# Performance work log

Measured on AMD Instinct MI355X. Metric: run time of the kernel, lower is better.

The kernel has to match this reference:

```python
import jax, jax.numpy as jnp
import numpy as np

NUM_HEADS = 12
KEEP_RATE = 0.7


def setup_inputs() -> dict:
    key = jax.random.key(0)
    ks = jax.random.split(key, 5)
    B, N, C = 64, 197, 768
    x = jax.random.normal(ks[0], (B, N, C), dtype=jnp.float32)
    qkv_w = jax.random.normal(ks[1], (3 * C, C), dtype=jnp.float32) * (C ** -0.5)
    qkv_b = jax.random.normal(ks[2], (3 * C,), dtype=jnp.float32) * 0.02
    proj_w = jax.random.normal(ks[3], (C, C), dtype=jnp.float32) * (C ** -0.5)
    proj_b = jax.random.normal(ks[4], (C,), dtype=jnp.float32) * 0.02
    return {"x": x, "qkv_w": qkv_w, "qkv_b": qkv_b, "proj_w": proj_w, "proj_b": proj_b}


def reference(x, qkv_w, qkv_b, proj_w, proj_b):
    B, N, C = x.shape
    H = NUM_HEADS
    D = C // H
    scale = D ** -0.5
    # qkv projection: [B,N,3C] -> [3,B,H,N,D]
    qkv = (x @ qkv_w.T + qkv_b).reshape(B, N, 3, H, D).transpose(2, 0, 3, 1, 4)
    q, k, v = qkv[0], qkv[1], qkv[2]
    # full materialized attention (required for cls-row extraction)
    attn = jax.nn.softmax(jnp.einsum('bhqd,bhkd->bhqk', q, k) * scale, axis=-1)
    out = jnp.einsum('bhqk,bhkd->bqhd', attn, v).reshape(B, N, C)
    out = out @ proj_w.T + proj_b
    # EViT token pruning: cls-token attention over non-cls keys, head-averaged
    left_tokens = int(KEEP_RATE * (N - 1))  # 137
    cls_attn = attn[:, :, 0, 1:].mean(axis=1)  # [B, N-1]
    _, idx = jax.lax.top_k(cls_attn, left_tokens)  # sorted descending, like torch.topk
    index = jnp.broadcast_to(idx[:, :, None], (B, left_tokens, C))
    return (out, index, idx, cls_attn)
```

## Files before the change

### kernel.cpp

```cpp
#include <hip/hip_runtime.h>
#include <hip/hip_bf16.h>
#include <stdint.h>

constexpr int BATCH = 64;
constexpr int NTOK  = 197;
constexpr int CDIM  = 768;
constexpr int NH    = 12;
constexpr int HD    = 64;
constexpr int MROWS = BATCH * NTOK;
constexpr int MPAD  = 12800;
constexpr int NROWT = MPAD / 128;
constexpr int LEFT  = 137;
constexpr int KPAD  = 224;
constexpr int BH    = BATCH * NH;
constexpr int SPAD  = 208;

constexpr size_t OUT_OFF_OUT   = 0;
constexpr size_t OUT_OFF_INDEX = (size_t)BATCH * NTOK * CDIM;
constexpr size_t OUT_OFF_IDX   = OUT_OFF_INDEX + (size_t)BATCH * LEFT * CDIM;
constexpr size_t OUT_OFF_CLS   = OUT_OFF_IDX + (size_t)BATCH * LEFT;

constexpr size_t WS_CLSPH = 0;
constexpr size_t WS_CLSF  = WS_CLSPH + (size_t)BH * (NTOK - 1);
constexpr size_t WS_IDXI  = WS_CLSF  + (size_t)BATCH * (NTOK - 1);
constexpr size_t WS_Q0    = WS_IDXI  + (size_t)BATCH * LEFT;
constexpr size_t WS_XB    = WS_Q0  + (size_t)BATCH * CDIM;
constexpr size_t WS_WB    = WS_XB  + (size_t)MPAD * CDIM / 2;
constexpr size_t WS_PB    = WS_WB  + (size_t)3 * CDIM * CDIM / 2;
constexpr size_t WS_QB    = WS_PB  + (size_t)CDIM * CDIM / 2;
constexpr size_t WS_KB    = WS_QB  + (size_t)BH * NTOK * HD / 2;
constexpr size_t WS_VTB   = WS_KB  + (size_t)BH * NTOK * HD / 2;
constexpr size_t WS_AOB   = WS_VTB + (size_t)BH * HD * KPAD / 2;
constexpr size_t WS_U     = WS_AOB + (size_t)MPAD * CDIM / 2;
constexpr size_t WS_S     = WS_U   + (size_t)BH * CDIM;

typedef __attribute__((ext_vector_type(8))) short short8;
typedef __attribute__((ext_vector_type(4))) float floatx4;

__device__ __forceinline__ ushort f2bf(float x) {
    __hip_bfloat16 h = __float2bfloat16(x);
    return *(ushort*)&h;
}

__device__ __forceinline__ void load_lds16(const ushort* g, ushort* l) {
    __builtin_amdgcn_global_load_lds(
        (const __attribute__((address_space(1))) uint32_t*)(uintptr_t)g,
        (__attribute__((address_space(3))) uint32_t*)(uint32_t)(uintptr_t)l,
        16, 0, 0);
}

constexpr int X_N4  = MROWS * CDIM / 4;
constexpr int X_NP4 = MPAD * CDIM / 4;
constexpr int W_N4  = 3 * CDIM * CDIM / 4;
constexpr int P_N4  = CDIM * CDIM / 4;
constexpr int CAST_TOTAL = X_NP4 + W_N4 + P_N4;
constexpr int CASTB = CAST_TOTAL / 256;

__global__ __launch_bounds__(256) void prep_kernel(const float* __restrict__ x,
                                                   const float* __restrict__ qkv_w,
                                                   const float* __restrict__ proj_w,
                                                   const float* __restrict__ qkv_b,
                                                   ushort* __restrict__ xb,
                                                   ushort* __restrict__ wb,
                                                   ushort* __restrict__ pb,
                                                   float* __restrict__ U,
                                                   float* __restrict__ qbW) {
    const int bk = blockIdx.x;
    const int t  = threadIdx.x;

    if (bk < CASTB) {
        const int i = bk * 256 + t;
        const float* src; ushort* dst; int j, valid;
        if (i < X_NP4)             { src = x;      dst = xb; j = i;                valid = (j < X_N4); }
        else if (i < X_NP4 + W_N4) { src = qkv_w;  dst = wb; j = i - X_NP4;        valid = 1; }
        else                       { src = proj_w; dst = pb; j = i - X_NP4 - W_N4; valid = 1; }
        ushort4 h4 = make_ushort4(0, 0, 0, 0);
        if (valid) {
            float4 a = ((const float4*)src)[j];
            h4 = make_ushort4(f2bf(a.x), f2bf(a.y), f2bf(a.z), f2bf(a.w));
        }
        ((ushort4*)dst)[j] = h4;
        return;
    }

    const int bh = bk - CASTB;
    const int b  = bh / NH;
    const int h  = bh - b * NH;
    const int wv   = t >> 6;
    const int lane = t & 63;

    __shared__ float x0s[CDIM];
    __shared__ float q0s[HD];

    if (t < 192) ((float4*)x0s)[t] = ((const float4*)(x + (size_t)b * NTOK * CDIM))[t];
    __syncthreads();

    for (int i = 0; i < 16; ++i) {
        const int cl = wv * 16 + i;
        const int c  = h * HD + cl;
        const float* wr = qkv_w + (size_t)c * CDIM;
        float s = 0.f;
#pragma unroll
        for (int k = 0; k < 3; ++k) {
            float4 xv  = *(const float4*)(x0s + lane * 4 + k * 256);
            float4 wv4 = *(const float4*)(wr  + lane * 4 + k * 256);
            s += xv.x * wv4.x + xv.y * wv4.y + xv.z * wv4.z + xv.w * wv4.w;
        }
#pragma unroll
        for (int off = 32; off >= 1; off >>= 1) s += __shfl_xor(s, off);
        if (lane == 0) q0s[cl] = s + qkv_b[c];
    }
    __syncthreads();

    if (wv == 0) {
        float p = q0s[lane] * qkv_b[CDIM + h * HD + lane];
#pragma unroll
        for (int off = 32; off >= 1; off >>= 1) p += __shfl_xor(p, off);
        if (lane == 0) qbW[bh] = p;
    }

    const float* wk = qkv_w + (size_t)(CDIM + h * HD) * CDIM;
    float a0 = 0.f, a1 = 0.f, a2 = 0.f;
    for (int d = 0; d < HD; d++) {
        const float qd = q0s[d];
        const float* row = wk + (size_t)d * CDIM;
        a0 = fmaf(qd, row[t],       a0);
        a1 = fmaf(qd, row[t + 256], a1);
        a2 = fmaf(qd, row[t + 512], a2);
    }
    float* ub = U + (size_t)bh * CDIM;
    ub[t] = a0; ub[t + 256] = a1; ub[t + 512] = a2;
}

__global__ __launch_bounds__(512) void score_kernel(const float* __restrict__ x,
                                                    const float* __restrict__ U,
                                                    float* __restrict__ S) {
    const int b    = blockIdx.y;
    const int wv   = threadIdx.x >> 6;
    const int lane = threadIdx.x & 63;

    __shared__ float Us[NH][CDIM];
    for (int i = threadIdx.x; i < NH * (CDIM / 4); i += 512)
        ((float4*)Us)[i] = ((const float4*)(U + (size_t)b * NH * CDIM))[i];
    __syncthreads();

    const int j = blockIdx.x * 8 + wv;
    if (j >= NTOK) return;

    const float* xr = x + ((size_t)b * NTOK + j) * CDIM;
    float4 xv[3];
#pragma unroll
    for (int i = 0; i < 3; i++) xv[i] = *(const float4*)(xr + lane * 4 + i * 256);

    for (int h = 0; h < NH; h++) {
        const float* ur = Us[h];
        float s = 0.f;
#pragma unroll
        for (int i = 0; i < 3; i++) {
            float4 uv = *(const float4*)(ur + lane * 4 + i * 256);
            s += xv[i].x * uv.x + xv[i].y * uv.y + xv[i].z * uv.z + xv[i].w * uv.w;
        }
#pragma unroll
        for (int off = 32; off >= 1; off >>= 1) s += __shfl_xor(s, off);
        if (lane == 0) S[(size_t)(b * NH + h) * SPAD + j] = s;
    }
}

constexpr int FILLB    = 256;
constexpr int FILL_TOT = BATCH * LEFT * (CDIM / 4);

template <int MODE, int NCOLT, bool DOFILL>
__global__ __launch_bounds__(256, 4) void mfma_gemm128(
    const ushort* __restrict__ A, const ushort* __restrict__ W,
    const float* __restrict__ bias,
    float* __restrict__ O0f, ushort* __restrict__ O0q,
    ushort* __restrict__ O1k, ushort* __restrict__ O2vd,
    const int* __restrict__ idxI, float* __restrict__ fillDst,
    int Mvalid, int N) {
    constexpr int K   = CDIM;
    constexpr int BK  = 32;
    constexpr int NTK = K / BK;
    constexpr int nwg = NROWT * NCOLT;
    __shared__ ushort sA[2 * 128 * BK];
    __shared__ ushort sB[2 * 128 * BK];

    if (DOFILL && blockIdx.x >= nwg) {
        const int fb = blockIdx.x - nwg;
        for (int i = fb * 256 + (int)threadIdx.x; i < FILL_TOT; i += FILLB * 256) {
            const float v = (float)idxI[i / (CDIM / 4)];
            ((float4*)fillDst)[i] = make_float4(v, v, v, v);
        }
        return;
    }

    const int t    = threadIdx.x;
    const int lane = t & 63;
    const int w    = t >> 6;
    const int wm   = (w >> 1) * 64;
    const int wn   = (w & 1) * 64;
    const int fr   = lane & 15;
    const int fq   = lane >> 4;
    const int f3   = lane & 3;

    int row, col;
    {
        constexpr int q = nwg >> 3, r = nwg & 7;
        const int xcd = blockIdx.x & 7, lin = blockIdx.x >> 3;
        const int wg = (xcd < r ? xcd * (q + 1) : r * (q + 1) + (xcd - r) * q) + lin;
        row = wg / NCOLT; col = wg - row * NCOLT;
    }
    const int rowBase = row * 128;
    const int colBase = col * 128;

    auto stage = [&](const ushort* __restrict__ G, ushort* dst, int grow0, int kt) {
#pragma unroll
        for (int i = 0; i < 2; ++i) {
            const int l  = i * 256 + t;
            const int rl = l >> 2;
            const int sl = (l & 3) ^ (rl & 3);
            load_lds16(G + (size_t)(grow0 + rl) * K + kt * BK + sl * 8,
                       dst + l * 8);
        }
    };

    floatx4 acc[4][4];
#pragma unroll
    for (int i = 0; i < 4; ++i)
#pragma unroll
        for (int j = 0; j < 4; ++j)
#pragma unroll
            for (int r2 = 0; r2 < 4; ++r2) acc[i][j][r2] = 0.f;

    const int s0 = (fq ^ f3) * 8;

    stage(A, sA, rowBase, 0);
    stage(W, sB, colBase, 0);

    for (int kt = 0; kt < NTK; ++kt) {
        __syncthreads();
        const int cb = (kt & 1) << 12;
        if (kt + 1 < NTK) {
            stage(A, sA + (cb ^ 4096), rowBase, kt + 1);
            stage(W, sB + (cb ^ 4096), colBase, kt + 1);
        }

        const ushort* pa = sA + cb + (wm + fr) * BK;
        const ushort* pb = sB + cb + (wn + fr) * BK;
        short8 af[4], bf[4];
#pragma unroll
        for (int i = 0; i < 4; ++i) {
            af[i] = *(const short8*)(pa + i * 512 + s0);
            bf[i] = *(const short8*)(pb + i * 512 + s0);
        }
#pragma unroll
        for (int i = 0; i < 4; ++i)
#pragma unroll
            for (int j = 0; j < 4; ++j)
                acc[i][j] = __builtin_amdgcn_mfma_f32_16x16x32_bf16(
                    af[i], bf[j], acc[i][j], 0, 0, 0);
    }

#pragma unroll
    for (int j = 0; j < 4; ++j) {
        const int nn = colBase + wn + j * 16 + fr;
        const float bq = bias[nn];
        if (MODE == 0) {
#pragma unroll
            for (int i = 0; i < 4; ++i) {
                const int mb = rowBase + wm + i * 16 + fq * 4;
#pragma unroll
                for (int r2 = 0; r2 < 4; ++r2) {
                    const int mm = mb + r2;
                    if (mm < Mvalid) O0f[(size_t)mm * N + nn] = acc[i][j][r2] + bq;
                }
            }
        } else {
            const int which = nn / CDIM;
            const int nc    = nn - which * CDIM;
            const int h     = nc >> 6;
            const int d     = nc & 63;
#pragma unroll
            for (int i = 0; i < 4; ++i) {
                const int mb = rowBase + wm + i * 16 + fq * 4;
#pragma unroll
                for (int r2 = 0; r2 < 4; ++r2) {
                    const int mm = mb + r2;
                    if (mm < Mvalid) {
                        const int b   = mm / NTOK;
                        const int tok = mm - b * NTOK;
                        const int bh  = b * NH + h;
                        const ushort val = f2bf(acc[i][j][r2] + bq);
                        if (which == 0)      O0q[((size_t)bh * NTOK + tok) * HD + d] = val;
                        else if (which == 1) O1k[((size_t)bh * NTOK + tok) * HD + d] = val;
                        else                 O2vd[(size_t)mm * CDIM + nc] = val;
                    }
                }
            }
        }
    }
}

__global__ __launch_bounds__(256) void attn_mfma_kernel(const ushort* __restrict__ Qb,
                                                        const ushort* __restrict__ Kb,
                                                        const ushort* __restrict__ Vd,
                                                        ushort* __restrict__ AOb) {
    const int bh = blockIdx.x;
    const int b  = bh / NH;
    const int h  = bh - b * NH;
    const int t  = threadIdx.x;
    const int wv   = t >> 6;
    const int lane = t & 63;
    const int qc   = lane & 15;
    const int quad = lane >> 4;

    constexpr int VSTR = KPAD + 8;
    __shared__ ushort Vt[HD][VSTR];
    __shared__ ushort Pl[4][4][16][32];
    __shared__ float  alf[4][4][16], lf[4][4][16];

    {
        for (int idx = t; idx < NTOK * 8; idx += 256) {
            const int tok = idx >> 3;
            const int d0  = (idx & 7) * 8;
            const short8 v = *(const short8*)(
                Vd + ((size_t)(b * NTOK + tok)) * CDIM + h * HD + d0);
#pragma unroll
            for (int jj = 0; jj < 8; ++jj) Vt[d0 + jj][tok] = (ushort)v[jj];
        }
        for (int idx = t; idx < (KPAD - NTOK) * HD; idx += 256) {
            const int tok = NTOK + (idx >> 6);
            const int d   = idx & 63;
            Vt[d][tok] = 0;
        }
    }

    const ushort* Qh = Qb + (size_t)bh * NTOK * HD;
    const ushort* Kh = Kb + (size_t)bh * NTOK * HD;

    const int tile0 = (wv == 0) ? 0 : 4 + (wv - 1) * 3;
    const int ntv   = (wv == 0) ? 4 : 3;

    short8 qf[4][2];
#pragma unroll
    for (int ti = 0; ti < 4; ++ti) {
        if (ti < ntv) {
            const int qrow = min((tile0 + ti) * 16 + qc, NTOK - 1);
            qf[ti][0] = *(const short8*)(Qh + (size_t)qrow * HD + quad * 8);
            qf[ti][1] = *(const short8*)(Qh + (size_t)qrow * HD + 32 + quad * 8);
        }
    }

    floatx4 o[4][4];
#pragma unroll
    for (int ti = 0; ti < 4; ++ti)
#pragma unroll
        for (int s = 0; s < 4; ++s)
#pragma unroll
            for (int r = 0; r < 4; ++r) o[ti][s][r] = 0.f;
    float m[4], l[4];
#pragma unroll
    for (int ti = 0; ti < 4; ++ti) { m[ti] = -INFINITY; l[ti] = 0.f; }

    __syncthreads();

    for (int c0 = 0; c0 < NTOK; c0 += 32) {
        const int kr0 = min(c0 + qc, NTOK - 1);
        const int kr1 = min(c0 + 16 + qc, NTOK - 1);
        const short8 kf00 = *(const short8*)(Kh + (size_t)kr0 * HD + quad * 8);
        const short8 kf01 = *(const short8*)(Kh + (size_t)kr0 * HD + 32 + quad * 8);
        const short8 kf10 = *(const short8*)(Kh + (size_t)kr1 * HD + quad * 8);
        const short8 kf11 = *(const short8*)(Kh + (size_t)kr1 * HD + 32 + quad * 8);

#pragma unroll
        for (int ti = 0; ti < 4; ++ti) {
            if (ti >= ntv) continue;
            floatx4 s0 = {0.f, 0.f, 0.f, 0.f}, s1 = {0.f, 0.f, 0.f, 0.f};
            s0 = __builtin_amdgcn_mfma_f32_16x16x32_bf16(kf00, qf[ti][0], s0, 0, 0, 0);
            s0 = __builtin_amdgcn_mfma_f32_16x16x32_bf16(kf01, qf[ti][1], s0, 0, 0, 0);
            s1 = __builtin_amdgcn_mfma_f32_16x16x32_bf16(kf10, qf[ti][0], s1, 0, 0, 0);
            s1 = __builtin_amdgcn_mfma_f32_16x16x32_bf16(kf11, qf[ti][1], s1, 0, 0, 0);

            float sv[8];
            float mloc = -INFINITY;
#pragma unroll
            for (int r = 0; r < 4; ++r) {
                const int key0 = c0 + quad * 4 + r;
                const int key1 = key0 + 16;
                sv[r]     = (key0 < NTOK) ? s0[r] * 0.125f : -1e30f;
                sv[4 + r] = (key1 < NTOK) ? s1[r] * 0.125f : -1e30f;
                mloc = fmaxf(mloc, fmaxf(sv[r], sv[4 + r]));
            }
            mloc = fmaxf(mloc, __shfl_xor(mloc, 16));
            mloc = fmaxf(mloc, __shfl_xor(mloc, 32));
            const float mnew  = fmaxf(m[ti], mloc);
            const float alpha = __expf(m[ti] - mnew);
            float p[8], ps = 0.f;
#pragma unroll
            for (int i = 0; i < 8; ++i) { p[i] = __expf(sv[i] - mnew); ps += p[i]; }
            ps += __shfl_xor(ps, 16);
            ps += __shfl_xor(ps, 32);
            l[ti] = l[ti] * alpha + ps;
            m[ti] = mnew;

#pragma unroll
            for (int r = 0; r < 4; ++r) {
                Pl[wv][ti][qc][quad * 4 + r]      = f2bf(p[r]);
                Pl[wv][ti][qc][16 + quad * 4 + r] = f2bf(p[4 + r]);
            }
            if (quad == 0) alf[wv][ti][qc] = alpha;
        }
        __syncthreads();

        short8 pf[4];
#pragma unroll
        for (int ti = 0; ti < 4; ++ti) {
            if (ti >= ntv) continue;
            pf[ti] = *(const short8*)&Pl[wv][ti][qc][quad * 8];
            float ar[4];
#pragma unroll
            for (int r = 0; r < 4; ++r) ar[r] = alf[wv][ti][quad * 4 + r];
#pragma unroll
            for (int s = 0; s < 4; ++s)
#pragma unroll
                for (int r = 0; r < 4; ++r) o[ti][s][r] *= ar[r];
        }

#pragma unroll
        for (int s = 0; s < 4; ++s) {
            const short8 vf = *(const short8*)&Vt[s * 16 + qc][c0 + quad * 8];
#pragma unroll
            for (int ti = 0; ti < 4; ++ti)
                if (ti < ntv)
                    o[ti][s] = __builtin_amdgcn_mfma_f32_16x16x32_bf16(
                        pf[ti], vf, o[ti][s], 0, 0, 0);
        }
        __syncthreads();
    }

#pragma unroll
    for (int ti = 0; ti < 4; ++ti)
        if (ti < ntv && quad == 0) lf[wv][ti][qc] = l[ti];
    __syncthreads();

#pragma unroll
    for (int ti = 0; ti < 4; ++ti) {
        if (ti >= ntv) continue;
        const int qt = tile0 + ti;
#pragma unroll
        for (int r = 0; r < 4; ++r) {
            const int tok = qt * 16 + quad * 4 + r;
            if (tok >= NTOK) continue;
            const float inv = 1.f / lf[wv][ti][quad * 4 + r];
            ushort* dst = AOb + ((size_t)(b * NTOK + tok)) * CDIM + h * HD;
#pragma unroll
            for (int s = 0; s < 4; ++s) dst[s * 16 + qc] = f2bf(o[ti][s][r] * inv);
        }
    }
}

__global__ __launch_bounds__(256) void topk_fused_kernel(const float* __restrict__ S,
                                                         const float* __restrict__ qbW,
                                                         int* __restrict__ idxI,
                                                         float* __restrict__ idxOut,
                                                         float* __restrict__ outCls) {
    const int b    = blockIdx.x;
    const int t    = threadIdx.x;
    const int lane = t & 63;
    const int w    = t >> 6;

    __shared__ float qbv[NH];
    __shared__ float redm[4], reds[4];
    __shared__ float vsh[NTOK - 1];

    if (t < NH) qbv[t] = qbW[b * NH + t];
    __syncthreads();

    float macc = 0.f;
    for (int h = 0; h < NH; ++h) {
        const float qb = qbv[h];
        const float sv = (t < NTOK) ? (S[(size_t)(b * NH + h) * SPAD + t] + qb) * 0.125f
                                    : -INFINITY;
        float mloc = sv;
#pragma unroll
        for (int off = 32; off >= 1; off >>= 1) mloc = fmaxf(mloc, __shfl_xor(mloc, off));
        if (lane == 0) redm[w] = mloc;
        __syncthreads();
        const float mx = fmaxf(fmaxf(redm[0], redm[1]), fmaxf(redm[2], redm[3]));
        const float p = (t < NTOK) ? expf(sv - mx) : 0.f;
        float ls = p;
#pragma unroll
        for (int off = 32; off >= 1; off >>= 1) ls += __shfl_xor(ls, off);
        if (lane == 0) reds[w] = ls;
        __syncthreads();
        const float denom = (reds[0] + reds[1]) + (reds[2] + reds[3]);
        macc += p / denom;
        __syncthreads();
    }

    if (t >= 1 && t < NTOK) {
        const float val = macc * (1.f / 12.f);
        vsh[t - 1] = val;
        outCls[(size_t)b * (NTOK - 1) + (t - 1)] = val;
    }
    __syncthreads();

    if (t < NTOK - 1) {
        const float vi = vsh[t];
        int rank = 0;
        for (int j = 0; j < NTOK - 1; j++) {
            const float vj = vsh[j];
            rank += (vj > vi) || (vj == vi && j < t);
        }
        if (rank < LEFT) {
            idxI[b * LEFT + rank]   = t;
            idxOut[b * LEFT + rank] = (float)t;
        }
    }
}

extern "C" void kernel_launch(void* const* d_in, const int* in_sizes, int n_in,
                              void* d_out, int out_size, void* d_ws, size_t ws_size,
                              hipStream_t stream) {
    const float* x      = (const float*)d_in[0];
    const float* qkv_w  = (const float*)d_in[1];
    const float* qkv_b  = (const float*)d_in[2];
    const float* proj_w = (const float*)d_in[3];
    const float* proj_b = (const float*)d_in[4];
    float* out = (float*)d_out;

    float*  ws    = (float*)d_ws;
    int*    idxi  = (int*)(ws + WS_IDXI);
    float*  qbW   = ws + WS_Q0;
    ushort* xb    = (ushort*)(ws + WS_XB);
    ushort* wb    = (ushort*)(ws + WS_WB);
    ushort* pb    = (ushort*)(ws + WS_PB);
    ushort* qb    = (ushort*)(ws + WS_QB);
    ushort* kb    = (ushort*)(ws + WS_KB);
    ushort* vd    = (ushort*)(ws + WS_VTB);
    ushort* aob   = (ushort*)(ws + WS_AOB);
    float*  U     = ws + WS_U;
    float*  S     = ws + WS_S;

    prep_kernel<<<CASTB + BH, 256, 0, stream>>>(x, qkv_w, proj_w, qkv_b,
                                                xb, wb, pb, U, qbW);

    score_kernel<<<dim3((NTOK + 7) / 8, BATCH), 512, 0, stream>>>(x, U, S);

    topk_fused_kernel<<<BATCH, 256, 0, stream>>>(S, qbW, idxi,
                                                 out + OUT_OFF_IDX,
                                                 out + OUT_OFF_CLS);

    mfma_gemm128<1, 18, true><<<NROWT * 18 + FILLB, 256, 0, stream>>>(
        xb, wb, qkv_b, nullptr, qb, kb, vd,
        idxi, out + OUT_OFF_INDEX, MROWS, 3 * CDIM);

    attn_mfma_kernel<<<BH, 256, 0, stream>>>(qb, kb, vd, aob);

    mfma_gemm128<0, 6, false><<<NROWT * 6, 256, 0, stream>>>(
        aob, pb, proj_b, out + OUT_OFF_OUT, nullptr, nullptr, nullptr,
        nullptr, nullptr, MROWS, CDIM);
}
```

Measured before the change: 330.5 us.

## Stage QKV GEMM epilogue through LDS for vectorized stores; move fill to attention

The QKV GEMM epilogue now writes its bias-added bf16 tile into shared memory, then emits 16-byte vector stores per head row (Q/K) or per token row (V), replacing scattered 2-byte stores. The index-broadcast fill blocks move from the QKV GEMM launch to the attention kernel launch, so they overlap attention instead of the GEMM. This adds two barriers per half-tile and reuses the GEMM's shared buffer for the staging transpose.

```diff
diff --git a/kernel.cpp b/kernel.cpp
--- a/kernel.cpp
+++ b/kernel.cpp
@@ -166,32 +166,20 @@
     }
 }
 
-constexpr int FILLB    = 256;
-constexpr int FILL_TOT = BATCH * LEFT * (CDIM / 4);
-
-template <int MODE, int NCOLT, bool DOFILL>
+template <int MODE, int NCOLT>
 __global__ __launch_bounds__(256, 4) void mfma_gemm128(
     const ushort* __restrict__ A, const ushort* __restrict__ W,
     const float* __restrict__ bias,
     float* __restrict__ O0f, ushort* __restrict__ O0q,
     ushort* __restrict__ O1k, ushort* __restrict__ O2vd,
-    const int* __restrict__ idxI, float* __restrict__ fillDst,
     int Mvalid, int N) {
     constexpr int K   = CDIM;
     constexpr int BK  = 32;
     constexpr int NTK = K / BK;
     constexpr int nwg = NROWT * NCOLT;
-    __shared__ ushort sA[2 * 128 * BK];
-    __shared__ ushort sB[2 * 128 * BK];
-
-    if (DOFILL && blockIdx.x >= nwg) {
-        const int fb = blockIdx.x - nwg;
-        for (int i = fb * 256 + (int)threadIdx.x; i < FILL_TOT; i += FILLB * 256) {
-            const float v = (float)idxI[i / (CDIM / 4)];
-            ((float4*)fillDst)[i] = make_float4(v, v, v, v);
-        }
-        return;
-    }
+    __shared__ ushort smem[16384];
+    ushort* sA = smem;
+    ushort* sB = smem + 8192;
 
     const int t    = threadIdx.x;
     const int lane = t & 63;
@@ -260,11 +248,11 @@
                     af[i], bf[j], acc[i][j], 0, 0, 0);
     }
 
-#pragma unroll
-    for (int j = 0; j < 4; ++j) {
-        const int nn = colBase + wn + j * 16 + fr;
-        const float bq = bias[nn];
-        if (MODE == 0) {
+    if (MODE == 0) {
+#pragma unroll
+        for (int j = 0; j < 4; ++j) {
+            const int nn = colBase + wn + j * 16 + fr;
+            const float bq = bias[nn];
 #pragma unroll
             for (int i = 0; i < 4; ++i) {
                 const int mb = rowBase + wm + i * 16 + fq * 4;
@@ -274,36 +262,79 @@
                     if (mm < Mvalid) O0f[(size_t)mm * N + nn] = acc[i][j][r2] + bq;
                 }
             }
-        } else {
-            const int which = nn / CDIM;
-            const int nc    = nn - which * CDIM;
-            const int h     = nc >> 6;
-            const int d     = nc & 63;
-#pragma unroll
-            for (int i = 0; i < 4; ++i) {
-                const int mb = rowBase + wm + i * 16 + fq * 4;
-#pragma unroll
-                for (int r2 = 0; r2 < 4; ++r2) {
-                    const int mm = mb + r2;
+        }
+    } else {
+        const int which = colBase / CDIM;
+        const int nc0   = colBase - which * CDIM;
+        const int hbase = nc0 >> 6;
+        ushort (*T)[136] = (ushort (*)[136])smem;
+        const int hpw = wm >> 6;
+#pragma unroll
+        for (int hp = 0; hp < 2; ++hp) {
+            __syncthreads();
+            if (hpw == hp) {
+#pragma unroll
+                for (int j = 0; j < 4; ++j) {
+                    const int nl = wn + j * 16 + fr;
+                    const float bq = bias[colBase + nl];
+#pragma unroll
+                    for (int i = 0; i < 4; ++i)
+#pragma unroll
+                        for (int r2 = 0; r2 < 4; ++r2)
+                            T[i * 16 + fq * 4 + r2][nl] = f2bf(acc[i][j][r2] + bq);
+                }
+            }
+            __syncthreads();
+            const int rowH = rowBase + hp * 64;
+            if (which < 2) {
+                ushort* O = (which == 0) ? O0q : O1k;
+#pragma unroll
+                for (int it = 0; it < 4; ++it) {
+                    const int run = it * 32 + (t >> 3);
+                    const int lr  = run >> 1;
+                    const int hh  = run & 1;
+                    const int d0  = (t & 7) * 8;
+                    const int mm  = rowH + lr;
                     if (mm < Mvalid) {
                         const int b   = mm / NTOK;
                         const int tok = mm - b * NTOK;
-                        const int bh  = b * NH + h;
-                        const ushort val = f2bf(acc[i][j][r2] + bq);
-                        if (which == 0)      O0q[((size_t)bh * NTOK + tok) * HD + d] = val;
-                        else if (which == 1) O1k[((size_t)bh * NTOK + tok) * HD + d] = val;
-                        else                 O2vd[(size_t)mm * CDIM + nc] = val;
+                        *(short8*)(O + (((size_t)(b * NH + hbase + hh) * NTOK + tok) * HD + d0)) =
+                            *(const short8*)&T[lr][hh * 64 + d0];
                     }
                 }
+            } else {
+#pragma unroll
+                for (int it = 0; it < 4; ++it) {
+                    const int lr = it * 16 + (t >> 4);
+                    const int c8 = (t & 15) * 8;
+                    const int mm = rowH + lr;
+                    if (mm < Mvalid)
+                        *(short8*)(O2vd + ((size_t)mm * CDIM + nc0 + c8)) =
+                            *(const short8*)&T[lr][c8];
+                }
             }
         }
     }
 }
+
+constexpr int FILLB    = 256;
+constexpr int FILL_TOT = BATCH * LEFT * (CDIM / 4);
 
 __global__ __launch_bounds__(256) void attn_mfma_kernel(const ushort* __restrict__ Qb,
                                                         const ushort* __restrict__ Kb,
                                                         const ushort* __restrict__ Vd,
-                                                        ushort* __restrict__ AOb) {
+                                                        ushort* __restrict__ AOb,
+                                                        const int* __restrict__ idxI,
+                                                        float* __restrict__ fillDst) {
+    if (blockIdx.x >= BH) {
+        const int fb = blockIdx.x - BH;
+        for (int i = fb * 256 + (int)threadIdx.x; i < FILL_TOT; i += FILLB * 256) {
+            const float v = (float)idxI[i / (CDIM / 4)];
+            ((float4*)fillDst)[i] = make_float4(v, v, v, v);
+        }
+        return;
+    }
+
     const int bh = blockIdx.x;
     const int b  = bh / NH;
     const int h  = bh - b * NH;
@@ -550,13 +581,13 @@
                                                  out + OUT_OFF_IDX,
                                                  out + OUT_OFF_CLS);
 
-    mfma_gemm128<1, 18, true><<<NROWT * 18 + FILLB, 256, 0, stream>>>(
-        xb, wb, qkv_b, nullptr, qb, kb, vd,
-        idxi, out + OUT_OFF_INDEX, MROWS, 3 * CDIM);
-
-    attn_mfma_kernel<<<BH, 256, 0, stream>>>(qb, kb, vd, aob);
-
-    mfma_gemm128<0, 6, false><<<NROWT * 6, 256, 0, stream>>>(
+    mfma_gemm128<1, 18><<<NROWT * 18, 256, 0, stream>>>(
+        xb, wb, qkv_b, nullptr, qb, kb, vd, MROWS, 3 * CDIM);
+
+    attn_mfma_kernel<<<BH + FILLB, 256, 0, stream>>>(qb, kb, vd, aob,
+                                                     idxi, out + OUT_OFF_INDEX);
+
+    mfma_gemm128<0, 6><<<NROWT * 6, 256, 0, stream>>>(
         aob, pb, proj_b, out + OUT_OFF_OUT, nullptr, nullptr, nullptr,
-        nullptr, nullptr, MROWS, CDIM);
-}
+        MROWS, CDIM);
+}
```

After: 303.5 us. 8.2% less time.
